# Optimization experiments

Hardware: AMD Instinct MI355X
Metric: run time of the kernel (lower is better)

The kernel has to match this reference:

```python
import jax, jax.numpy as jnp
import numpy as np

K = 2            # num_classes (fixed in module)
THRESH = 0.01    # CdistThreshold
MAX_ITERS = 3    # loop breaks when Ci > 3 -> at most 3 work iterations


def _l2norm(x, eps=1e-12):
    # torch F.normalize(dim=1) on [N, C]-style rows -> normalize last axis here
    n = jnp.linalg.norm(x, axis=-1, keepdims=True)
    return x / jnp.maximum(n, eps)


def _step(feats, centers):
    """One k-means iteration, vectorized over batch.
    feats:   [B, N, C]  centers: [K, C]
    Returns (new_centers [K,C], CurDist scalar, labels [B,N])."""
    B = feats.shape[0]
    fn = _l2norm(feats)
    cn = _l2norm(centers)
    # cosine distance 0.5*(1 - cos_sim): [B, N, K]
    dists = 0.5 * (1.0 - jnp.einsum('bnc,kc->bnk', fn, cn))
    labels = jnp.argmin(dists, axis=-1)                      # [B, N]
    mask = jax.nn.one_hot(labels, K, dtype=feats.dtype)      # [B, N, K]
    sums = jnp.einsum('bnc,bnk->bkc', feats, mask)           # [B, K, C]
    counts = jnp.sum(mask, axis=1)                           # [B, K]
    centers_iter = sums / (counts[..., None] + 1.0)          # [B, K, C] (note +1 as in torch)
    # per-batch mean cosine similarity between new per-batch centers and old centers
    num = jnp.sum(centers_iter * centers[None], axis=-1)     # [B, K]
    den = jnp.maximum(
        jnp.linalg.norm(centers_iter, axis=-1) * jnp.linalg.norm(centers, axis=-1)[None],
        1e-8)
    cdist = jnp.mean(num / den, axis=-1)                     # [B]
    new_centers = jnp.sum(centers_iter, axis=0) / B          # centersIterout / B
    cur_dist = jnp.sum(cdist) / B                            # CdistT / B
    return new_centers, cur_dist, labels


def setup_inputs() -> dict:
    key = jax.random.key(0)
    k1, k2 = jax.random.split(key)
    FeatureT = jax.random.normal(k1, (8, 256, 256, 256), dtype=jnp.float32)
    centerInit = jax.random.normal(k2, (K, 256), dtype=jnp.float32)
    return {"FeatureT": FeatureT, "centerInit": centerInit}


def reference(FeatureT, centerInit):
    B, C = FeatureT.shape[0], FeatureT.shape[1]
    feats = FeatureT.reshape(B, C, -1).transpose(0, 2, 1)    # [B, N, C]
    # iteration 1 always runs (centers = centerInit)
    centers, cur_dist, labels = _step(feats, centerInit)
    done = cur_dist < THRESH
    # iterations 2..3, frozen once converged (matches the while-loop break)
    for _ in range(MAX_ITERS - 1):
        nc, cd, lb = _step(feats, centers)
        centers = jnp.where(done, centers, nc)
        labels = jnp.where(done, labels, lb)
        cur_dist = jnp.where(done, cur_dist, cd)
        done = done | (cur_dist < THRESH)
    labels_onehot = jax.nn.one_hot(labels.reshape(-1), K, dtype=jnp.float32)  # [B*N, K]
    # torch returns centersIterout.detach()
    return jax.lax.stop_gradient(centers), labels, labels_onehot, cur_dist
```

## Files before the change

### kernel.cpp

```cpp
#include <hip/hip_runtime.h>
#include <stdint.h>

#define CDIM   256
#define NPIX   65536
#define NBATCH 8
#define WCOLS  64
#define NTILES 1024
#define TPB    16
#define NBLOCKS (NBATCH * NTILES / TPB)
#define KTHRESH 0.01

#define WS_DELTA 0
#define WS_CENT  256
#define WS_T     768
#define WS_S1    2816
#define WS_CNT   4864
#define WS_DONE  4872

#define OUT_LABELS 512
#define OUT_ONEHOT (512 + NBATCH * NPIX)
#define OUT_CDIST  (512 + NBATCH * NPIX + 2 * NBATCH * NPIX)

#define TILE_WORDS 16664

__device__ __forceinline__ void dma_row4(const float* g, float* l) {
  __builtin_amdgcn_global_load_lds((const __attribute__((address_space(1))) void*)g,
                                   (__attribute__((address_space(3))) void*)l, 4, 0, 0);
}

__device__ __forceinline__ double block_reduce(double v, double* sh) {
  const int t = threadIdx.x;
  #pragma unroll
  for (int off = 32; off > 0; off >>= 1) v += __shfl_down(v, off, 64);
  __syncthreads();
  if ((t & 63) == 0) sh[t >> 6] = v;
  __syncthreads();
  return sh[0] + sh[1] + sh[2] + sh[3];
}

__device__ __forceinline__ void block_reduce4(double v[4], double* sh) {
  const int t = threadIdx.x;
  #pragma unroll
  for (int off = 32; off > 0; off >>= 1) {
    v[0] += __shfl_down(v[0], off, 64);
    v[1] += __shfl_down(v[1], off, 64);
    v[2] += __shfl_down(v[2], off, 64);
    v[3] += __shfl_down(v[3], off, 64);
  }
  __syncthreads();
  if ((t & 63) == 0) {
    const int w = t >> 6;
    sh[w] = v[0]; sh[4 + w] = v[1]; sh[8 + w] = v[2]; sh[12 + w] = v[3];
  }
  __syncthreads();
  #pragma unroll
  for (int k = 0; k < 4; ++k) v[k] = sh[4 * k] + sh[4 * k + 1] + sh[4 * k + 2] + sh[4 * k + 3];
}

__global__ __launch_bounds__(256) void init_kernel(const float* __restrict__ cinit,
                                                   float* __restrict__ ws) {
  __shared__ double sh[16];
  const int t = threadIdx.x;
  for (int i = t; i < NBATCH * CDIM; i += 256) { ws[WS_T + i] = 0.f; ws[WS_S1 + i] = 0.f; }
  if (t < NBATCH) ((unsigned int*)(ws + WS_CNT))[t] = 0u;
  if (t == 0) ((int*)(ws + WS_DONE))[0] = 0;
  const float c0f = cinit[t], c1f = cinit[CDIM + t];
  ws[WS_CENT + t] = c0f;
  ws[WS_CENT + CDIM + t] = c1f;
  const double c0 = (double)c0f, c1 = (double)c1f;
  double n0 = sqrt(block_reduce(c0 * c0, sh));
  double n1 = sqrt(block_reduce(c1 * c1, sh));
  n0 = fmax(n0, 1e-12); n1 = fmax(n1, 1e-12);
  ws[WS_DELTA + t] = (float)(c1 / n1) - (float)(c0 / n0);
}

__global__ __launch_bounds__(256, 1) void pass_kernel(const float* __restrict__ F,
                                                      float* __restrict__ ws,
                                                      float* __restrict__ out,
                                                      int iter) {
  if (iter > 0 && ((const volatile int*)(ws + WS_DONE))[0] != 0) return;

  __shared__ float tile[2][TILE_WORDS];
  __shared__ float deltaS[4 * 72];

  const int t  = threadIdx.x;
  const int w  = t >> 6;
  const int l  = t & 63;
  const int b  = blockIdx.x >> 6;
  const int tile0 = (blockIdx.x & 63) * TPB;

  if (t < CDIM) deltaS[(t >> 6) * 72 + (t & 63)] = ws[WS_DELTA + t];

  const float* Fb = F + (size_t)b * CDIM * NPIX;

  {
    const size_t g0 = (size_t)(tile0 * WCOLS) + l;
    #pragma unroll
    for (int r = 0; r < 64; ++r) {
      const int c = w * 64 + r;
      dma_row4(Fb + (size_t)c * NPIX + g0, &tile[0][65 * c + 8 * (c >> 6) + l]);
    }
  }

  float s1[4] = {0.f, 0.f, 0.f, 0.f};
  float tv[4] = {0.f, 0.f, 0.f, 0.f};
  unsigned cnt = 0;

  const int cseg = l >> 4;
  const int q    = l & 15;
  const int nloc = w * 16 + q;

  int buf = 0;
  for (int i = 0; i < TPB; ++i) {
    asm volatile("s_waitcnt vmcnt(0)" ::: "memory");
    __syncthreads();

    if (i + 1 < TPB) {
      const size_t g0 = (size_t)((tile0 + i + 1) * WCOLS) + l;
      float* dst = tile[buf ^ 1];
      #pragma unroll
      for (int r = 0; r < 64; ++r) {
        const int c = w * 64 + r;
        dma_row4(Fb + (size_t)c * NPIX + g0, &dst[65 * c + 8 * (c >> 6) + l]);
      }
    }

    const float* T = tile[buf];

    double d = 0.0;
    const float* Tcol = T + (size_t)(cseg * 64) * 65 + 8 * cseg + nloc;
    const float* dl = deltaS + cseg * 72;
    #pragma unroll
    for (int j = 0; j < 64; ++j)
      d = fma((double)dl[j], (double)Tcol[(size_t)j * 65], d);
    d += __shfl_down(d, 32, 64);
    d += __shfl_down(d, 16, 64);
    const unsigned long long ball = __ballot(d > 0.0);
    const unsigned mask16 = (unsigned)(ball & 0xFFFFull);
    cnt += __popc(mask16);

    const int n0 = (tile0 + i) * WCOLS;
    if (l < 16) {
      const float m = (float)((mask16 >> l) & 1u);
      const int gi = b * NPIX + n0 + w * 16 + l;
      out[OUT_LABELS + gi] = m;
      ((float2*)(out + OUT_ONEHOT))[gi] = make_float2(1.0f - m, m);
    }

    #pragma unroll
    for (int k = 0; k < 4; ++k) {
      const float* row = T + (size_t)(l + 64 * k) * 65 + 8 * k + w * 16;
      float a1 = 0.f, at = 0.f;
      #pragma unroll
      for (int qq = 0; qq < 16; ++qq) {
        const float v = row[qq];
        a1 = fmaf((float)((mask16 >> qq) & 1u), v, a1);
        at += v;
      }
      s1[k] += a1;
      tv[k] += at;
    }
    buf ^= 1;
  }

  #pragma unroll
  for (int k = 0; k < 4; ++k) {
    unsafeAtomicAdd(&ws[WS_S1 + b * CDIM + l + 64 * k], s1[k]);
    if (iter == 0) unsafeAtomicAdd(&ws[WS_T + b * CDIM + l + 64 * k], tv[k]);
  }
  if (l == 0) atomicAdd(&((unsigned int*)(ws + WS_CNT))[b], cnt);
}

__global__ __launch_bounds__(256) void finalize_kernel(float* __restrict__ ws,
                                                       float* __restrict__ out) {
  __shared__ double sh[16];
  const int t = threadIdx.x;
  if (((const volatile int*)(ws + WS_DONE))[0] != 0) return;

  const double cold0 = (double)ws[WS_CENT + t];
  const double cold1 = (double)ws[WS_CENT + CDIM + t];
  const double normc0 = sqrt(block_reduce(cold0 * cold0, sh));
  const double normc1 = sqrt(block_reduce(cold1 * cold1, sh));

  double acc0 = 0.0, acc1 = 0.0, cdsum = 0.0;
  for (int b = 0; b < NBATCH; ++b) {
    const double s1v  = (double)ws[WS_S1 + b * CDIM + t];
    const double totv = (double)ws[WS_T  + b * CDIM + t];
    const double c1n  = (double)((unsigned int*)(ws + WS_CNT))[b];
    const double ci1  = s1v / (c1n + 1.0);
    const double ci0  = (totv - s1v) / ((double)NPIX - c1n + 1.0);
    acc0 += ci0; acc1 += ci1;
    double v[4] = {ci0 * cold0, ci0 * ci0, ci1 * cold1, ci1 * ci1};
    block_reduce4(v, sh);
    const double den0 = fmax(sqrt(v[1]) * normc0, 1e-8);
    const double den1 = fmax(sqrt(v[3]) * normc1, 1e-8);
    cdsum += 0.5 * (v[0] / den0 + v[2] / den1);
  }
  const double curdist = cdsum / (double)NBATCH;
  const float nc0f = (float)(acc0 / (double)NBATCH);
  const float nc1f = (float)(acc1 / (double)NBATCH);

  ws[WS_CENT + t] = nc0f;
  ws[WS_CENT + CDIM + t] = nc1f;
  out[t] = nc0f;
  out[CDIM + t] = nc1f;
  if (t == 0) out[OUT_CDIST] = (float)curdist;

  double m0 = sqrt(block_reduce((double)nc0f * (double)nc0f, sh));
  double m1 = sqrt(block_reduce((double)nc1f * (double)nc1f, sh));
  m0 = fmax(m0, 1e-12); m1 = fmax(m1, 1e-12);
  ws[WS_DELTA + t] = (float)((double)nc1f / m1) - (float)((double)nc0f / m0);

  __syncthreads();
  for (int i = t; i < NBATCH * CDIM; i += 256) ws[WS_S1 + i] = 0.f;
  if (t < NBATCH) ((unsigned int*)(ws + WS_CNT))[t] = 0u;
  if (t == 0) ((int*)(ws + WS_DONE))[0] = (curdist < KTHRESH) ? 1 : 0;
}

extern "C" void kernel_launch(void* const* d_in, const int* in_sizes, int n_in,
                              void* d_out, int out_size, void* d_ws, size_t ws_size,
                              hipStream_t stream) {
  const float* F     = (const float*)d_in[0];
  const float* cinit = (const float*)d_in[1];
  float* out = (float*)d_out;
  float* ws  = (float*)d_ws;

  init_kernel<<<1, 256, 0, stream>>>(cinit, ws);
  for (int iter = 0; iter < 3; ++iter) {
    pass_kernel<<<NBLOCKS, 256, 0, stream>>>(F, ws, out, iter);
    finalize_kernel<<<1, 256, 0, stream>>>(ws, out);
  }
}
```

Baseline: 1.135 ms.

## Replace LDS DMA tiling with register-resident float4 loads and LDS cross-wave reduction

The pass kernel no longer stages 64x256 feature tiles into LDS with global_load_lds. Each thread now loads 16 channels x 4 pixels as float4 straight into registers, double-buffered in registers. Per-pixel distance partials are reduced through shuffles plus a small LDS array, and per-channel sums are reduced with shuffles before the atomics. This removes the large LDS footprint so two blocks can share a CU, and widens the global loads. In exchange it uses many more registers, adds a __syncthreads per tile, and leaves latency hiding to the register prefetch and the extra occupancy.

Result: slower. 1.224 ms (+7.8%).

```diff
diff --git a/kernel.cpp b/kernel.cpp
--- a/kernel.cpp
+++ b/kernel.cpp
@@ -20,13 +20,6 @@
 #define OUT_LABELS 512
 #define OUT_ONEHOT (512 + NBATCH * NPIX)
 #define OUT_CDIST  (512 + NBATCH * NPIX + 2 * NBATCH * NPIX)
-
-#define TILE_WORDS 16664
-
-__device__ __forceinline__ void dma_row4(const float* g, float* l) {
-  __builtin_amdgcn_global_load_lds((const __attribute__((address_space(1))) void*)g,
-                                   (__attribute__((address_space(3))) void*)l, 4, 0, 0);
-}
 
 __device__ __forceinline__ double block_reduce(double v, double* sh) {
   const int t = threadIdx.x;
@@ -74,101 +67,121 @@
   ws[WS_DELTA + t] = (float)(c1 / n1) - (float)(c0 / n0);
 }
 
-__global__ __launch_bounds__(256, 1) void pass_kernel(const float* __restrict__ F,
+__global__ __launch_bounds__(256, 2) void pass_kernel(const float* __restrict__ F,
                                                       float* __restrict__ ws,
                                                       float* __restrict__ out,
                                                       int iter) {
   if (iter > 0 && ((const volatile int*)(ws + WS_DONE))[0] != 0) return;
 
-  __shared__ float tile[2][TILE_WORDS];
-  __shared__ float deltaS[4 * 72];
-
-  const int t  = threadIdx.x;
-  const int w  = t >> 6;
-  const int l  = t & 63;
-  const int b  = blockIdx.x >> 6;
+  __shared__ double pd[2][4][16][5];
+
+  const int t    = threadIdx.x;
+  const int w    = t >> 6;
+  const int l    = t & 63;
+  const int cg   = l & 15;
+  const int rgrp = l >> 4;
+  const int b    = blockIdx.x >> 6;
   const int tile0 = (blockIdx.x & 63) * TPB;
-
-  if (t < CDIM) deltaS[(t >> 6) * 72 + (t & 63)] = ws[WS_DELTA + t];
-
-  const float* Fb = F + (size_t)b * CDIM * NPIX;
-
-  {
-    const size_t g0 = (size_t)(tile0 * WCOLS) + l;
-    #pragma unroll
-    for (int r = 0; r < 64; ++r) {
-      const int c = w * 64 + r;
-      dma_row4(Fb + (size_t)c * NPIX + g0, &tile[0][65 * c + 8 * (c >> 6) + l]);
-    }
-  }
-
-  float s1[4] = {0.f, 0.f, 0.f, 0.f};
-  float tv[4] = {0.f, 0.f, 0.f, 0.f};
+  const int cbase = w * 64 + rgrp * 16;
+
+  float dreg[16];
+  #pragma unroll
+  for (int r = 0; r < 16; ++r) dreg[r] = ws[WS_DELTA + cbase + r];
+
+  const float* Fb = F + (size_t)b * CDIM * NPIX + (size_t)cbase * NPIX + (size_t)cg * 4;
+
+  float4 A[16], Bv[16];
+  float s1[16], tv[16];
+  #pragma unroll
+  for (int r = 0; r < 16; ++r) { s1[r] = 0.f; tv[r] = 0.f; }
   unsigned cnt = 0;
 
-  const int cseg = l >> 4;
-  const int q    = l & 15;
-  const int nloc = w * 16 + q;
-
-  int buf = 0;
-  for (int i = 0; i < TPB; ++i) {
-    asm volatile("s_waitcnt vmcnt(0)" ::: "memory");
+  auto load_tile = [&](float4* buf, int tile) {
+    const float* p = Fb + (size_t)tile * WCOLS;
+    #pragma unroll
+    for (int r = 0; r < 16; ++r)
+      buf[r] = *(const float4*)(p + (size_t)r * NPIX);
+  };
+
+  auto process = [&](const float4* V, int i) {
+    double d0 = 0.0, d1 = 0.0, d2 = 0.0, d3 = 0.0;
+    #pragma unroll
+    for (int r = 0; r < 16; ++r) {
+      const double dc = (double)dreg[r];
+      d0 = fma(dc, (double)V[r].x, d0);
+      d1 = fma(dc, (double)V[r].y, d1);
+      d2 = fma(dc, (double)V[r].z, d2);
+      d3 = fma(dc, (double)V[r].w, d3);
+    }
+    d0 += __shfl_xor(d0, 16, 64); d0 += __shfl_xor(d0, 32, 64);
+    d1 += __shfl_xor(d1, 16, 64); d1 += __shfl_xor(d1, 32, 64);
+    d2 += __shfl_xor(d2, 16, 64); d2 += __shfl_xor(d2, 32, 64);
+    d3 += __shfl_xor(d3, 16, 64); d3 += __shfl_xor(d3, 32, 64);
+    const int par = i & 1;
+    if (rgrp == 0) {
+      pd[par][w][cg][0] = d0; pd[par][w][cg][1] = d1;
+      pd[par][w][cg][2] = d2; pd[par][w][cg][3] = d3;
+    }
     __syncthreads();
-
-    if (i + 1 < TPB) {
-      const size_t g0 = (size_t)((tile0 + i + 1) * WCOLS) + l;
-      float* dst = tile[buf ^ 1];
-      #pragma unroll
-      for (int r = 0; r < 64; ++r) {
-        const int c = w * 64 + r;
-        dma_row4(Fb + (size_t)c * NPIX + g0, &dst[65 * c + 8 * (c >> 6) + l]);
-      }
-    }
-
-    const float* T = tile[buf];
-
-    double d = 0.0;
-    const float* Tcol = T + (size_t)(cseg * 64) * 65 + 8 * cseg + nloc;
-    const float* dl = deltaS + cseg * 72;
-    #pragma unroll
-    for (int j = 0; j < 64; ++j)
-      d = fma((double)dl[j], (double)Tcol[(size_t)j * 65], d);
-    d += __shfl_down(d, 32, 64);
-    d += __shfl_down(d, 16, 64);
-    const unsigned long long ball = __ballot(d > 0.0);
-    const unsigned mask16 = (unsigned)(ball & 0xFFFFull);
-    cnt += __popc(mask16);
-
-    const int n0 = (tile0 + i) * WCOLS;
-    if (l < 16) {
-      const float m = (float)((mask16 >> l) & 1u);
-      const int gi = b * NPIX + n0 + w * 16 + l;
-      out[OUT_LABELS + gi] = m;
-      ((float2*)(out + OUT_ONEHOT))[gi] = make_float2(1.0f - m, m);
-    }
-
-    #pragma unroll
-    for (int k = 0; k < 4; ++k) {
-      const float* row = T + (size_t)(l + 64 * k) * 65 + 8 * k + w * 16;
-      float a1 = 0.f, at = 0.f;
-      #pragma unroll
-      for (int qq = 0; qq < 16; ++qq) {
-        const float v = row[qq];
-        a1 = fmaf((float)((mask16 >> qq) & 1u), v, a1);
-        at += v;
-      }
-      s1[k] += a1;
-      tv[k] += at;
-    }
-    buf ^= 1;
-  }
-
-  #pragma unroll
-  for (int k = 0; k < 4; ++k) {
-    unsafeAtomicAdd(&ws[WS_S1 + b * CDIM + l + 64 * k], s1[k]);
-    if (iter == 0) unsafeAtomicAdd(&ws[WS_T + b * CDIM + l + 64 * k], tv[k]);
-  }
-  if (l == 0) atomicAdd(&((unsigned int*)(ws + WS_CNT))[b], cnt);
+    const double f0 = pd[par][0][cg][0] + pd[par][1][cg][0] + pd[par][2][cg][0] + pd[par][3][cg][0];
+    const double f1 = pd[par][0][cg][1] + pd[par][1][cg][1] + pd[par][2][cg][1] + pd[par][3][cg][1];
+    const double f2 = pd[par][0][cg][2] + pd[par][1][cg][2] + pd[par][2][cg][2] + pd[par][3][cg][2];
+    const double f3 = pd[par][0][cg][3] + pd[par][1][cg][3] + pd[par][2][cg][3] + pd[par][3][cg][3];
+    const float m0 = f0 > 0.0 ? 1.f : 0.f;
+    const float m1 = f1 > 0.0 ? 1.f : 0.f;
+    const float m2 = f2 > 0.0 ? 1.f : 0.f;
+    const float m3 = f3 > 0.0 ? 1.f : 0.f;
+
+    if (w == 0 && rgrp == 0) {
+      const int gi = b * NPIX + (tile0 + i) * WCOLS + cg * 4;
+      *(float4*)(out + OUT_LABELS + gi) = make_float4(m0, m1, m2, m3);
+      float4* oh = (float4*)(out + OUT_ONEHOT + 2 * (size_t)gi);
+      oh[0] = make_float4(1.f - m0, m0, 1.f - m1, m1);
+      oh[1] = make_float4(1.f - m2, m2, 1.f - m3, m3);
+      cnt += (unsigned)(m0 + m1 + m2 + m3);
+    }
+
+    #pragma unroll
+    for (int r = 0; r < 16; ++r) {
+      const float4 v = V[r];
+      float a = fmaf(m0, v.x, s1[r]);
+      a = fmaf(m1, v.y, a);
+      a = fmaf(m2, v.z, a);
+      s1[r] = fmaf(m3, v.w, a);
+      tv[r] += (v.x + v.y) + (v.z + v.w);
+    }
+  };
+
+  load_tile(A, tile0);
+  for (int i = 0; i < TPB; i += 2) {
+    load_tile(Bv, tile0 + i + 1);
+    process(A, i);
+    if (i + 2 < TPB) load_tile(A, tile0 + i + 2);
+    process(Bv, i + 1);
+  }
+
+  #pragma unroll
+  for (int r = 0; r < 16; ++r) {
+    #pragma unroll
+    for (int m = 1; m < 16; m <<= 1) {
+      s1[r] += __shfl_xor(s1[r], m, 64);
+      tv[r] += __shfl_xor(tv[r], m, 64);
+    }
+  }
+  if (cg == 0) {
+    #pragma unroll
+    for (int r = 0; r < 16; ++r) {
+      unsafeAtomicAdd(&ws[WS_S1 + b * CDIM + cbase + r], s1[r]);
+      if (iter == 0) unsafeAtomicAdd(&ws[WS_T + b * CDIM + cbase + r], tv[r]);
+    }
+  }
+  if (w == 0 && rgrp == 0) {
+    cnt += __shfl_down(cnt, 8, 16);
+    cnt += __shfl_down(cnt, 4, 16);
+    cnt += __shfl_down(cnt, 2, 16);
+    cnt += __shfl_down(cnt, 1, 16);
+    if (cg == 0) atomicAdd(&((unsigned int*)(ws + WS_CNT))[b], cnt);
+  }
 }
 
 __global__ __launch_bounds__(256) void finalize_kernel(float* __restrict__ ws,
```
